# Performance work log

Hardware: AMD Instinct MI355X
Metric: run time of the kernel (lower is better)

Reference implementation:

```python
import jax, jax.numpy as jnp
import numpy as np

L, H, D, V, TMAX = 12, 12, 768, 50257, 1024
B, T = 2, 1024
HD = D // H
EPS = 1e-5


def new_gelu(x):
    return 0.5 * x * (1.0 + jnp.tanh(jnp.sqrt(2.0 / jnp.pi) * (x + 0.044715 * x ** 3)))


def layer_norm(x, w, b):
    mu = jnp.mean(x, axis=-1, keepdims=True)
    var = jnp.var(x, axis=-1, keepdims=True)
    return (x - mu) * jax.lax.rsqrt(var + EPS) * w + b


def setup_inputs() -> dict:
    key = jax.random.key(0)
    ks = jax.random.split(key, 12)
    s = 0.02
    return {
        "idx": jax.random.randint(ks[0], (B, T), 0, V),
        "wte": jax.random.normal(ks[1], (V, D), jnp.float32) * s,
        "wpe": jax.random.normal(ks[2], (TMAX, D), jnp.float32) * s,
        "ln1_w": jnp.ones((L, D), jnp.float32),
        "ln1_b": jnp.zeros((L, D), jnp.float32),
        "attn_w": jax.random.normal(ks[3], (L, D, 3 * D), jnp.float32) * s,
        "attn_b": jnp.zeros((L, 3 * D), jnp.float32),
        "proj_w": jax.random.normal(ks[4], (L, D, D), jnp.float32) * (s / jnp.sqrt(2.0 * L)),
        "proj_b": jnp.zeros((L, D), jnp.float32),
        "ln2_w": jnp.ones((L, D), jnp.float32),
        "ln2_b": jnp.zeros((L, D), jnp.float32),
        "fc_w": jax.random.normal(ks[5], (L, D, 4 * D), jnp.float32) * s,
        "fc_b": jnp.zeros((L, 4 * D), jnp.float32),
        "fc2_w": jax.random.normal(ks[6], (L, 4 * D, D), jnp.float32) * (s / jnp.sqrt(2.0 * L)),
        "fc2_b": jnp.zeros((L, D), jnp.float32),
        "lnf_w": jnp.ones((D,), jnp.float32),
        "lnf_b": jnp.zeros((D,), jnp.float32),
        "lm_head_w": jax.random.normal(ks[7], (D, V), jnp.float32) * s,
    }


def _gpt_forward(idx, wte, wpe, ln1_w, ln1_b, attn_w, attn_b, proj_w, proj_b,
                 ln2_w, ln2_b, fc_w, fc_b, fc2_w, fc2_b, lnf_w, lnf_b, lm_head_w):
    b, t = idx.shape
    x = wte[idx] + wpe[:t][None, :, :]  # [B,T,D]
    causal = jnp.tril(jnp.ones((t, t), bool))  # [T,T]
    scale = 1.0 / jnp.sqrt(jnp.asarray(HD, x.dtype))

    layer_params = {
        "ln1_w": ln1_w, "ln1_b": ln1_b, "attn_w": attn_w, "attn_b": attn_b,
        "proj_w": proj_w, "proj_b": proj_b, "ln2_w": ln2_w, "ln2_b": ln2_b,
        "fc_w": fc_w, "fc_b": fc_b, "fc2_w": fc2_w, "fc2_b": fc2_b,
    }

    def block(x, p):
        h = layer_norm(x, p["ln1_w"], p["ln1_b"])
        qkv = h @ p["attn_w"] + p["attn_b"]  # [B,T,3D]
        q, k, v = jnp.split(qkv, 3, axis=-1)
        q = q.reshape(b, t, H, HD)
        k = k.reshape(b, t, H, HD)
        v = v.reshape(b, t, H, HD)
        att = jnp.einsum("bqhd,bkhd->bhqk", q, k) * scale
        att = jnp.where(causal[None, None, :, :], att, -jnp.inf)
        att = jax.nn.softmax(att, axis=-1)
        y = jnp.einsum("bhqk,bkhd->bqhd", att, v).reshape(b, t, D)
        x = x + y @ p["proj_w"] + p["proj_b"]
        h2 = layer_norm(x, p["ln2_w"], p["ln2_b"])
        m = new_gelu(h2 @ p["fc_w"] + p["fc_b"])
        x = x + m @ p["fc2_w"] + p["fc2_b"]
        return x, None

    x, _ = jax.lax.scan(block, x, layer_params)
    x = layer_norm(x, lnf_w, lnf_b)
    logits = x @ lm_head_w  # [B,T,V]
    return logits


def reference(idx, wte, wpe, ln1_w, ln1_b, attn_w, attn_b, proj_w, proj_b,
              ln2_w, ln2_b, fc_w, fc_b, fc2_w, fc2_b, lnf_w, lnf_b, lm_head_w):
    return _gpt_forward(idx, wte, wpe, ln1_w, ln1_b, attn_w, attn_b, proj_w, proj_b,
                        ln2_w, ln2_b, fc_w, fc_b, fc2_w, fc2_b, lnf_w, lnf_b, lm_head_w)
```

## Files before the change

kernel.cpp:

```cpp
#include <hip/hip_runtime.h>
#include <math.h>

#define Bsz  2
#define Tlen 1024
#define Dm   768
#define Hh   12
#define HDm  64
#define Ll   12
#define Vv   50257
#define Mrows (Bsz * Tlen)
#define WPL  7077888

typedef __attribute__((ext_vector_type(8))) short short8;
typedef __attribute__((ext_vector_type(4))) float f32x4;

__device__ __forceinline__ float bf2f(unsigned short u) {
  union { unsigned int i; float f; } v; v.i = ((unsigned int)u) << 16; return v.f;
}
__device__ __forceinline__ unsigned short f2bf(float f) {
  union { float f; unsigned int i; } v; v.f = f;
  unsigned int u = v.i;
  return (unsigned short)((u + 0x7FFFu + ((u >> 16) & 1u)) >> 16);
}
__device__ __forceinline__ float gelu_f(float x) {
  const float c = 0.7978845608028654f;
  return 0.5f * x * (1.0f + tanhf(c * (x + 0.044715f * x * x * x)));
}

__device__ __forceinline__ void gl_lds16(const unsigned short* g, unsigned short* l) {
  __builtin_amdgcn_global_load_lds(
      (const __attribute__((address_space(1))) unsigned int*)g,
      (__attribute__((address_space(3))) unsigned int*)l, 16, 0, 0);
}


__global__ void embed_kernel(const int* __restrict__ idx, const float* __restrict__ wte,
                             const float* __restrict__ wpe, float* __restrict__ x) {
  int i = (blockIdx.x * 256 + threadIdx.x) * 4;
  int d = i % Dm;
  int bt = i / Dm;
  int t = bt % Tlen;
  int tok = idx[bt];
  float4 a = *(const float4*)(wte + (size_t)tok * Dm + d);
  float4 p = *(const float4*)(wpe + (size_t)t * Dm + d);
  float4 r; r.x = a.x + p.x; r.y = a.y + p.y; r.z = a.z + p.z; r.w = a.w + p.w;
  *(float4*)(x + i) = r;
}

__global__ __launch_bounds__(256) void ln_wave(const float* __restrict__ x,
                                               const float* __restrict__ w,
                                               const float* __restrict__ b,
                                               unsigned short* __restrict__ out) {
  int tid = threadIdx.x, wv = tid >> 6, l = tid & 63;
  int row = blockIdx.x * 4 + wv;
  const float* xr = x + (size_t)row * Dm;
  float4 v[3];
  float s = 0.f, s2 = 0.f;
#pragma unroll
  for (int i = 0; i < 3; ++i) {
    v[i] = *(const float4*)(xr + l * 4 + i * 256);
    s += v[i].x + v[i].y + v[i].z + v[i].w;
    s2 += v[i].x * v[i].x + v[i].y * v[i].y + v[i].z * v[i].z + v[i].w * v[i].w;
  }
#pragma unroll
  for (int o = 1; o < 64; o <<= 1) {
    s += __shfl_xor(s, o, 64);
    s2 += __shfl_xor(s2, o, 64);
  }
  float mu = s * (1.0f / Dm);
  float var = s2 * (1.0f / Dm) - mu * mu;
  float rstd = rsqrtf(var + 1e-5f);
  unsigned short* yr = out + (size_t)row * Dm;
#pragma unroll
  for (int i = 0; i < 3; ++i) {
    float4 wv4 = *(const float4*)(w + l * 4 + i * 256);
    float4 bv4 = *(const float4*)(b + l * 4 + i * 256);
    ushort4 o4;
    o4.x = f2bf((v[i].x - mu) * rstd * wv4.x + bv4.x);
    o4.y = f2bf((v[i].y - mu) * rstd * wv4.y + bv4.y);
    o4.z = f2bf((v[i].z - mu) * rstd * wv4.z + bv4.z);
    o4.w = f2bf((v[i].w - mu) * rstd * wv4.w + bv4.w);
    *(ushort4*)(yr + l * 4 + i * 256) = o4;
  }
}

__global__ __launch_bounds__(256) void tconv_kernel(const float* __restrict__ W, int ldw,
                                                    int nValid, unsigned short* __restrict__ WT,
                                                    int K) {
  __shared__ float S[32][33];
  int n0 = blockIdx.x * 32, k0 = blockIdx.y * 32;
  int t = threadIdx.x;
  int nc = t & 31, kr0 = t >> 5;
#pragma unroll
  for (int i = 0; i < 4; ++i) {
    int kr = kr0 + i * 8;
    S[kr][nc] = (n0 + nc < nValid) ? W[(size_t)(k0 + kr) * ldw + n0 + nc] : 0.f;
  }
  __syncthreads();
  int r = t >> 3, c4 = (t & 7) * 4;
  ushort4 o;
  o.x = f2bf(S[c4 + 0][r]); o.y = f2bf(S[c4 + 1][r]);
  o.z = f2bf(S[c4 + 2][r]); o.w = f2bf(S[c4 + 3][r]);
  *(ushort4*)(WT + (size_t)(n0 + r) * K + k0 + c4) = o;
}

__global__ __launch_bounds__(256) void tconv12_kernel(
    const float* __restrict__ attn_w, const float* __restrict__ proj_w,
    const float* __restrict__ fc_w, const float* __restrict__ fc2_w,
    unsigned short* __restrict__ wAll) {
  int bid = blockIdx.x;
  int lyr = bid / 6912, rem = bid % 6912;
  unsigned short* wL = wAll + (size_t)lyr * WPL;
  const float* W; unsigned short* WT; int ldw, K, ntn, local;
  if (rem < 1728)      { W = attn_w + (size_t)lyr * Dm * 3 * Dm; WT = wL;                     ldw = 2304; K = 768;  ntn = 72; local = rem; }
  else if (rem < 2304) { W = proj_w + (size_t)lyr * Dm * Dm;     WT = wL + 1769472;           ldw = 768;  K = 768;  ntn = 24; local = rem - 1728; }
  else if (rem < 4608) { W = fc_w + (size_t)lyr * Dm * 4 * Dm;   WT = wL + 1769472 + 589824;  ldw = 3072; K = 768;  ntn = 96; local = rem - 2304; }
  else                 { W = fc2_w + (size_t)lyr * 4 * Dm * Dm;  WT = wL + 1769472 + 589824 + 2359296; ldw = 768; K = 3072; ntn = 24; local = rem - 4608; }
  int n0 = (local % ntn) * 32, k0 = (local / ntn) * 32;
  __shared__ float S[32][33];
  int t = threadIdx.x;
  int nc = t & 31, kr0 = t >> 5;
#pragma unroll
  for (int i = 0; i < 4; ++i) {
    int kr = kr0 + i * 8;
    S[kr][nc] = W[(size_t)(k0 + kr) * ldw + n0 + nc];
  }
  __syncthreads();
  int r = t >> 3, c4 = (t & 7) * 4;
  ushort4 o;
  o.x = f2bf(S[c4 + 0][r]); o.y = f2bf(S[c4 + 1][r]);
  o.z = f2bf(S[c4 + 2][r]); o.w = f2bf(S[c4 + 3][r]);
  *(ushort4*)(WT + (size_t)(n0 + r) * K + k0 + c4) = o;
}

template<bool XMAP>
__global__ __launch_bounds__(256) void gemm_big(
    const unsigned short* __restrict__ A, const unsigned short* __restrict__ B, int K,
    const float* __restrict__ bias, const float* __restrict__ res,
    float* __restrict__ outF, unsigned short* __restrict__ outB,
    int ldc, int nValid, int act, int nColTiles) {
  int brow, bcol;
  if (XMAP) {
    int b = blockIdx.x, xcd = b & 7, slot = b >> 3;
    bcol = xcd + 8 * (slot >> 4);
    brow = slot & 15;
    if (bcol >= nColTiles) return;
  } else {
    bcol = blockIdx.x; brow = blockIdx.y;
  }
  __shared__ alignas(16) unsigned short As[3][128][32];
  __shared__ alignas(16) unsigned short Bs[3][128][32];
  int tid = threadIdx.x;
  int rowBase = brow * 128, colBase = bcol * 128;
  int w = tid >> 6, l = tid & 63;
  int wr = w >> 1, wc = w & 1;
  int srow = tid >> 2;
  int skk = (((tid & 3) ^ ((tid >> 3) & 3))) * 8;
  const unsigned short* aSrc = A + (size_t)(rowBase + srow) * K + skk;
  const unsigned short* bSrc = B + (size_t)(colBase + srow) * K + skk;

  f32x4 acc[4][4];
#pragma unroll
  for (int m = 0; m < 4; ++m)
#pragma unroll
    for (int n = 0; n < 4; ++n) acc[m][n] = (f32x4){0.f, 0.f, 0.f, 0.f};

  int fr = l & 15, fq = l >> 4;
  int kslot = (fq ^ ((fr >> 1) & 3)) * 8;

#define STAGE_BIG(t_, buf_)                                              \
  { int k0_ = (t_) * 32;                                                 \
    gl_lds16(aSrc + k0_, &As[buf_][w * 16][0]);                          \
    gl_lds16(aSrc + (size_t)64 * K + k0_, &As[buf_][w * 16 + 64][0]);    \
    gl_lds16(bSrc + k0_, &Bs[buf_][w * 16][0]);                          \
    gl_lds16(bSrc + (size_t)64 * K + k0_, &Bs[buf_][w * 16 + 64][0]); }

  int nIt = K >> 5;
  STAGE_BIG(0, 0);
  STAGE_BIG(1, 1);

  int cur = 0;
  for (int it = 0; it < nIt; ++it) {
    if (it + 2 < nIt) {
      int nxt = cur + 2; if (nxt >= 3) nxt -= 3;
      STAGE_BIG(it + 2, nxt);
      asm volatile("s_waitcnt vmcnt(8)" ::: "memory");
    } else if (it + 1 < nIt) {
      asm volatile("s_waitcnt vmcnt(4)" ::: "memory");
    } else {
      asm volatile("s_waitcnt vmcnt(0)" ::: "memory");
    }
    asm volatile("s_barrier" ::: "memory");

    short8 af[4], bfr[4];
#pragma unroll
    for (int m = 0; m < 4; ++m)
      af[m] = *(const short8*)&As[cur][wr * 64 + m * 16 + fr][kslot];
#pragma unroll
    for (int n = 0; n < 4; ++n)
      bfr[n] = *(const short8*)&Bs[cur][wc * 64 + n * 16 + fr][kslot];
#pragma unroll
    for (int m = 0; m < 4; ++m)
#pragma unroll
      for (int n = 0; n < 4; ++n)
        acc[m][n] = __builtin_amdgcn_mfma_f32_16x16x32_bf16(af[m], bfr[n], acc[m][n], 0, 0, 0);
    asm volatile("s_barrier" ::: "memory");
    cur = cur + 1; if (cur >= 3) cur = 0;
  }
#undef STAGE_BIG

#pragma unroll
  for (int m = 0; m < 4; ++m) {
    int row = rowBase + wr * 64 + m * 16 + fq * 4;
#pragma unroll
    for (int n = 0; n < 4; ++n) {
      int col = colBase + wc * 64 + n * 16 + fr;
      if (col >= nValid) continue;
      float bv = bias ? bias[col] : 0.f;
#pragma unroll
      for (int j = 0; j < 4; ++j) {
        float v = acc[m][n][j] + bv;
        if (act) v = gelu_f(v);
        if (res) v += res[(size_t)(row + j) * ldc + col];
        if (outF) outF[(size_t)(row + j) * ldc + col] = v;
        else      outB[(size_t)(row + j) * ldc + col] = f2bf(v);
      }
    }
  }
}

__global__ __launch_bounds__(256) void gemm_bf16_sm(
    const unsigned short* __restrict__ A, const unsigned short* __restrict__ B, int K,
    const float* __restrict__ bias,
    float* __restrict__ outF, unsigned short* __restrict__ outB,
    int ldc, int act) {
  __shared__ alignas(16) unsigned short As[3][64][32];
  __shared__ alignas(16) unsigned short Bs[3][128][32];
  int tid = threadIdx.x;
  int rowBase = blockIdx.y * 64;
  int colBase = blockIdx.x * 128;
  int w = tid >> 6, l = tid & 63;
  int fr = l & 15, fq = l >> 4;

  int srow = l >> 2;
  int skk = (((l & 3) ^ ((l >> 3) & 3))) * 8;
  const unsigned short* aSrc = A + (size_t)(rowBase + w * 16 + srow) * K + skk;
  const unsigned short* bSrc = B + (size_t)(colBase + w * 16 + srow) * K + skk;
  int kslot = (fq ^ ((fr >> 1) & 3)) * 8;

  f32x4 acc[4][2];
#pragma unroll
  for (int m = 0; m < 4; ++m)
#pragma unroll
    for (int n = 0; n < 2; ++n) acc[m][n] = (f32x4){0.f, 0.f, 0.f, 0.f};

#define STAGE_SM(t_, buf_)                                               \
  { int k0_ = (t_) * 32;                                                 \
    gl_lds16(aSrc + k0_, &As[buf_][w * 16][0]);                          \
    gl_lds16(bSrc + k0_, &Bs[buf_][w * 16][0]);                          \
    gl_lds16(bSrc + (size_t)64 * K + k0_, &Bs[buf_][w * 16 + 64][0]); }

  int nIt = K >> 5;
  STAGE_SM(0, 0);
  STAGE_SM(1, 1);

  int cur = 0;
  for (int it = 0; it < nIt; ++it) {
    if (it + 2 < nIt) {
      int nxt = cur + 2; if (nxt >= 3) nxt -= 3;
      STAGE_SM(it + 2, nxt);
      asm volatile("s_waitcnt vmcnt(6)" ::: "memory");
    } else if (it + 1 < nIt) {
      asm volatile("s_waitcnt vmcnt(3)" ::: "memory");
    } else {
      asm volatile("s_waitcnt vmcnt(0)" ::: "memory");
    }
    asm volatile("s_barrier" ::: "memory");

    short8 af[4], bfr[2];
#pragma unroll
    for (int m = 0; m < 4; ++m)
      af[m] = *(const short8*)&As[cur][m * 16 + fr][kslot];
#pragma unroll
    for (int n = 0; n < 2; ++n)
      bfr[n] = *(const short8*)&Bs[cur][w * 32 + n * 16 + fr][kslot];
#pragma unroll
    for (int m = 0; m < 4; ++m)
#pragma unroll
      for (int n = 0; n < 2; ++n)
        acc[m][n] = __builtin_amdgcn_mfma_f32_16x16x32_bf16(af[m], bfr[n], acc[m][n], 0, 0, 0);
    asm volatile("s_barrier" ::: "memory");
    cur = cur + 1; if (cur >= 3) cur = 0;
  }
#undef STAGE_SM

#pragma unroll
  for (int m = 0; m < 4; ++m) {
    int row = rowBase + m * 16 + fq * 4;
#pragma unroll
    for (int n = 0; n < 2; ++n) {
      int col = colBase + w * 32 + n * 16 + fr;
      float bv = bias ? bias[col] : 0.f;
#pragma unroll
      for (int j = 0; j < 4; ++j) {
        float v = acc[m][n][j] + bv;
        if (act) v = gelu_f(v);
        if (outF) outF[(size_t)(row + j) * ldc + col] = v;
        else      outB[(size_t)(row + j) * ldc + col] = f2bf(v);
      }
    }
  }
}

__global__ __launch_bounds__(256) void gemm_splitk(
    const unsigned short* __restrict__ A, const unsigned short* __restrict__ B, int K,
    int Klen, const float* __restrict__ bias, float* __restrict__ outF, int ldc) {
  __shared__ alignas(16) unsigned short As[3][64][32];
  __shared__ alignas(16) unsigned short Bs[3][128][32];
  int tid = threadIdx.x;
  int rowBase = blockIdx.y * 64;
  int colBase = blockIdx.x * 128;
  int Koff = blockIdx.z * Klen;
  int w = tid >> 6, l = tid & 63;
  int fr = l & 15, fq = l >> 4;

  int srow = l >> 2;
  int skk = (((l & 3) ^ ((l >> 3) & 3))) * 8;
  const unsigned short* aSrc = A + (size_t)(rowBase + w * 16 + srow) * K + Koff + skk;
  const unsigned short* bSrc = B + (size_t)(colBase + w * 16 + srow) * K + Koff + skk;
  int kslot = (fq ^ ((fr >> 1) & 3)) * 8;

  f32x4 acc[4][2];
#pragma unroll
  for (int m = 0; m < 4; ++m)
#pragma unroll
    for (int n = 0; n < 2; ++n) acc[m][n] = (f32x4){0.f, 0.f, 0.f, 0.f};

#define STAGE_SK(t_, buf_)                                               \
  { int k0_ = (t_) * 32;                                                 \
    gl_lds16(aSrc + k0_, &As[buf_][w * 16][0]);                          \
    gl_lds16(bSrc + k0_, &Bs[buf_][w * 16][0]);                          \
    gl_lds16(bSrc + (size_t)64 * K + k0_, &Bs[buf_][w * 16 + 64][0]); }

  int nIt = Klen >> 5;
  STAGE_SK(0, 0);
  STAGE_SK(1, 1);

  int cur = 0;
  for (int it = 0; it < nIt; ++it) {
    if (it + 2 < nIt) {
      int nxt = cur + 2; if (nxt >= 3) nxt -= 3;
      STAGE_SK(it + 2, nxt);
      asm volatile("s_waitcnt vmcnt(6)" ::: "memory");
    } else if (it + 1 < nIt) {
      asm volatile("s_waitcnt vmcnt(3)" ::: "memory");
    } else {
      asm volatile("s_waitcnt vmcnt(0)" ::: "memory");
    }
    asm volatile("s_barrier" ::: "memory");

    short8 af[4], bfr[2];
#pragma unroll
    for (int m = 0; m < 4; ++m)
      af[m] = *(const short8*)&As[cur][m * 16 + fr][kslot];
#pragma unroll
    for (int n = 0; n < 2; ++n)
      bfr[n] = *(const short8*)&Bs[cur][w * 32 + n * 16 + fr][kslot];
#pragma unroll
    for (int m = 0; m < 4; ++m)
#pragma unroll
      for (int n = 0; n < 2; ++n)
        acc[m][n] = __builtin_amdgcn_mfma_f32_16x16x32_bf16(af[m], bfr[n], acc[m][n], 0, 0, 0);
    asm volatile("s_barrier" ::: "memory");
    cur = cur + 1; if (cur >= 3) cur = 0;
  }
#undef STAGE_SK

  bool addBias = (blockIdx.z == 0);
#pragma unroll
  for (int m = 0; m < 4; ++m) {
    int row = rowBase + m * 16 + fq * 4;
#pragma unroll
    for (int n = 0; n < 2; ++n) {
      int col = colBase + w * 32 + n * 16 + fr;
      float bv = addBias ? bias[col] : 0.f;
#pragma unroll
      for (int j = 0; j < 4; ++j) {
        unsafeAtomicAdd(&outF[(size_t)(row + j) * ldc + col], acc[m][n][j] + bv);
      }
    }
  }
}

__global__ __launch_bounds__(256) void attn_mfma(const unsigned short* __restrict__ qkv,
                                                 unsigned short* __restrict__ y) {
  int bx = blockIdx.x;
  int qt = 15 - (bx / 24);
  int bh = bx % 24;
  int h  = bh % Hh;
  int b  = bh / Hh;
  int q0 = qt * 64;
  int tid = threadIdx.x;
  int w = tid >> 6, l = tid & 63;
  int g = l >> 4, fr = l & 15;

  __shared__ alignas(16) unsigned short Kl[2][4096];
  __shared__ alignas(16) unsigned short Vt[4096];
  __shared__ alignas(16) unsigned short Pl[4][1024];

  const size_t rs = 3 * Dm;
  const unsigned short* base = qkv + (size_t)(b * Tlen) * rs + h * HDm;

  short8 qf[2];
  {
    const unsigned short* qrow = base + (size_t)(q0 + w * 16 + fr) * rs;
    qf[0] = *(const short8*)(qrow + g * 8);
    qf[1] = *(const short8*)(qrow + g * 8 + 32);
  }

  int vt_t = tid >> 2, vt_dc = tid & 3;
  uint4 v0r, v1r;

  f32x4 oAcc[4];
#pragma unroll
  for (int nd = 0; nd < 4; ++nd) oAcc[nd] = (f32x4){0.f, 0.f, 0.f, 0.f};
  float mRun[4] = {-1e30f, -1e30f, -1e30f, -1e30f};
  float lRun[4] = {0.f, 0.f, 0.f, 0.f};

  unsigned short* Pw = &Pl[w][0];
  int nkt = qt + 1;

  {
#pragma unroll
    for (int i = 0; i < 2; ++i) {
      int c = i * 256 + tid;
      int t = c >> 3, cl = c & 7;
      int dch = cl ^ (t & 7);
      gl_lds16(base + (size_t)t * rs + Dm + dch * 8, &Kl[0][(i * 256 + w * 64) * 8]);
    }
    const unsigned short* p = base + (size_t)vt_t * rs + 2 * Dm + vt_dc * 16;
    v0r = *(const uint4*)p;
    v1r = *(const uint4*)(p + 8);
  }

  for (int kt = 0; kt < nkt; ++kt) {
    int cur = kt & 1;
    int kbase = kt * 64;
    asm volatile("s_waitcnt vmcnt(0)" ::: "memory");
    __builtin_amdgcn_s_barrier();

    {
      union { uint4 u; unsigned short s[8]; } a, bb;
      a.u = v0r; bb.u = v1r;
#pragma unroll
      for (int j = 0; j < 8; ++j) {
        int d = vt_dc * 16 + j;
        Vt[d * 64 + (vt_t ^ ((d & 7) << 3))] = a.s[j];
        int d2 = d + 8;
        Vt[d2 * 64 + (vt_t ^ ((d2 & 7) << 3))] = bb.s[j];
      }
    }
    if (kt + 1 < nkt) {
      int kb = kbase + 64;
#pragma unroll
      for (int i = 0; i < 2; ++i) {
        int c = i * 256 + tid;
        int t = c >> 3, cl = c & 7;
        int dch = cl ^ (t & 7);
        gl_lds16(base + (size_t)(kb + t) * rs + Dm + dch * 8,
                 &Kl[cur ^ 1][(i * 256 + w * 64) * 8]);
      }
      const unsigned short* p = base + (size_t)(kb + vt_t) * rs + 2 * Dm + vt_dc * 16;
      v0r = *(const uint4*)p;
      v1r = *(const uint4*)(p + 8);
    }
    asm volatile("s_waitcnt lgkmcnt(0)" ::: "memory");
    __builtin_amdgcn_s_barrier();

    f32x4 sAcc[4];
#pragma unroll
    for (int nt = 0; nt < 4; ++nt) sAcc[nt] = (f32x4){0.f, 0.f, 0.f, 0.f};
#pragma unroll
    for (int ks = 0; ks < 2; ++ks)
#pragma unroll
      for (int nt = 0; nt < 4; ++nt) {
        int kcol = nt * 16 + fr;
        short8 kf = *(const short8*)&Kl[cur][kcol * 64 + ((g * 8 + ks * 32) ^ ((kcol & 7) << 3))];
        sAcc[nt] = __builtin_amdgcn_mfma_f32_16x16x32_bf16(qf[ks], kf, sAcc[nt], 0, 0, 0);
      }

    float corr[4];
#pragma unroll
    for (int j = 0; j < 4; ++j) {
      int qg = q0 + w * 16 + g * 4 + j;
      float tm = -1e30f;
#pragma unroll
      for (int nt = 0; nt < 4; ++nt) {
        float s = sAcc[nt][j] * 0.125f;
        int tg = kbase + nt * 16 + fr;
        if (tg > qg) s = -1e30f;
        sAcc[nt][j] = s;
        tm = fmaxf(tm, s);
      }
      tm = fmaxf(tm, __shfl_xor(tm, 1, 16));
      tm = fmaxf(tm, __shfl_xor(tm, 2, 16));
      tm = fmaxf(tm, __shfl_xor(tm, 4, 16));
      tm = fmaxf(tm, __shfl_xor(tm, 8, 16));
      float mN = fmaxf(mRun[j], tm);
      corr[j] = __expf(mRun[j] - mN);
      mRun[j] = mN;
      float ps = 0.f;
#pragma unroll
      for (int nt = 0; nt < 4; ++nt) {
        float p = __expf(sAcc[nt][j] - mN);
        sAcc[nt][j] = p;
        ps += p;
      }
      ps += __shfl_xor(ps, 1, 16);
      ps += __shfl_xor(ps, 2, 16);
      ps += __shfl_xor(ps, 4, 16);
      ps += __shfl_xor(ps, 8, 16);
      lRun[j] = lRun[j] * corr[j] + ps;
    }

#pragma unroll
    for (int nt = 0; nt < 4; ++nt)
#pragma unroll
      for (int j = 0; j < 4; ++j) {
        int q = g * 4 + j;
        int t = nt * 16 + fr;
        Pw[q * 64 + (t ^ ((q & 7) << 3))] = f2bf(sAcc[nt][j]);
      }
#pragma unroll
    for (int nd = 0; nd < 4; ++nd)
#pragma unroll
      for (int j = 0; j < 4; ++j) oAcc[nd][j] *= corr[j];

#pragma unroll
    for (int ks = 0; ks < 2; ++ks) {
      short8 pf = *(const short8*)&Pw[fr * 64 + ((g * 8 + ks * 32) ^ ((fr & 7) << 3))];
#pragma unroll
      for (int nd = 0; nd < 4; ++nd) {
        int d = nd * 16 + fr;
        short8 vf = *(const short8*)&Vt[d * 64 + ((g * 8 + ks * 32) ^ ((fr & 7) << 3))];
        oAcc[nd] = __builtin_amdgcn_mfma_f32_16x16x32_bf16(pf, vf, oAcc[nd], 0, 0, 0);
      }
    }
  }

#pragma unroll
  for (int j = 0; j < 4; ++j) {
    float inv = 1.0f / lRun[j];
    int q = q0 + w * 16 + g * 4 + j;
    unsigned short* yr = y + (size_t)(b * Tlen + q) * Dm + h * HDm + fr;
#pragma unroll
    for (int nd = 0; nd < 4; ++nd)
      yr[nd * 16] = f2bf(oAcc[nd][j] * inv);
  }
}

extern "C" void kernel_launch(void* const* d_in, const int* in_sizes, int n_in,
                              void* d_out, int out_size, void* d_ws, size_t ws_size,
                              hipStream_t stream) {
  const int*   idx    = (const int*)d_in[0];
  const float* wte    = (const float*)d_in[1];
  const float* wpe    = (const float*)d_in[2];
  const float* ln1_w  = (const float*)d_in[3];
  const float* ln1_b  = (const float*)d_in[4];
  const float* attn_w = (const float*)d_in[5];
  const float* attn_b = (const float*)d_in[6];
  const float* proj_w = (const float*)d_in[7];
  const float* proj_b = (const float*)d_in[8];
  const float* ln2_w  = (const float*)d_in[9];
  const float* ln2_b  = (const float*)d_in[10];
  const float* fc_w   = (const float*)d_in[11];
  const float* fc_b   = (const float*)d_in[12];
  const float* fc2_w  = (const float*)d_in[13];
  const float* fc2_b  = (const float*)d_in[14];
  const float* lnf_w  = (const float*)d_in[15];
  const float* lnf_b  = (const float*)d_in[16];
  const float* lmw    = (const float*)d_in[17];
  float* out = (float*)d_out;

  float* x = (float*)d_ws;
  unsigned short* qkvb = (unsigned short*)(x + (size_t)Mrows * Dm);
  unsigned short* xb   = qkvb + (size_t)Mrows * 3 * Dm;
  unsigned short* yb   = xb + (size_t)Mrows * Dm;
  unsigned short* mb   = yb + (size_t)Mrows * Dm;
  unsigned short* wbuf = mb + (size_t)Mrows * 4 * Dm;

  unsigned short* wAll = (unsigned short*)d_out;

  const size_t baseBytes = (size_t)Mrows * Dm * 4 + (size_t)Mrows * 9 * Dm * 2;
  size_t availShorts = (ws_size - baseBytes) / 2;
  long long cc = (long long)(availShorts / Dm) & ~127LL;
  if (cc > 50304) cc = 50304;
  const int chunkCols = (int)cc;

  embed_kernel<<<(Mrows * Dm) / 1024, 256, 0, stream>>>(idx, wte, wpe, x);
  tconv12_kernel<<<6912 * Ll, 256, 0, stream>>>(attn_w, proj_w, fc_w, fc2_w, wAll);

  for (int l = 0; l < Ll; ++l) {
    unsigned short* wL    = wAll + (size_t)l * WPL;
    unsigned short* wAttn = wL;
    unsigned short* wProj = wL + 1769472;
    unsigned short* wFc   = wL + 1769472 + 589824;
    unsigned short* wFc2  = wL + 1769472 + 589824 + 2359296;

    ln_wave<<<Mrows / 4, 256, 0, stream>>>(x, ln1_w + l * Dm, ln1_b + l * Dm, xb);
    gemm_bf16_sm<<<dim3(18, 32), 256, 0, stream>>>(xb, wAttn, Dm, attn_b + (size_t)l * 3 * Dm,
                                                   nullptr, qkvb, 3 * Dm, 0);
    attn_mfma<<<Bsz * Hh * 16, 256, 0, stream>>>(qkvb, yb);
    gemm_splitk<<<dim3(6, 32, 2), 256, 0, stream>>>(yb, wProj, Dm, Dm / 2,
                                                    proj_b + (size_t)l * Dm, x, Dm);
    ln_wave<<<Mrows / 4, 256, 0, stream>>>(x, ln2_w + l * Dm, ln2_b + l * Dm, xb);
    gemm_bf16_sm<<<dim3(24, 32), 256, 0, stream>>>(xb, wFc, Dm, fc_b + (size_t)l * 4 * Dm,
                                                   nullptr, mb, 4 * Dm, 1);
    gemm_splitk<<<dim3(6, 32, 2), 256, 0, stream>>>(mb, wFc2, 4 * Dm, 2 * Dm,
                                                    fc2_b + (size_t)l * Dm, x, Dm);
  }

  ln_wave<<<Mrows / 4, 256, 0, stream>>>(x, lnf_w, lnf_b, xb);
  for (int base = 0; base < Vv; base += chunkCols) {
    int ncv = Vv - base; if (ncv > chunkCols) ncv = chunkCols;
    int ntiles = (ncv + 127) / 128;
    tconv_kernel<<<dim3((ncv + 31) / 32, 24), 256, 0, stream>>>(lmw + base, Vv, ncv, wbuf, Dm);
    int cpx = (ntiles + 7) / 8;
    gemm_big<true><<<8 * 16 * cpx, 256, 0, stream>>>(
        xb, wbuf, Dm, nullptr, nullptr, out + base, nullptr, Vv, ncv, 0, ntiles);
  }
}
```

Before: 2.228 ms.

## Split causal attention over key ranges with merge kernel; single-barrier GEMM pipelines

```diff
diff --git a/kernel.cpp b/kernel.cpp
--- a/kernel.cpp
+++ b/kernel.cpp
@@ -181,16 +181,13 @@
 
   int cur = 0;
   for (int it = 0; it < nIt; ++it) {
+    if (it < nIt - 1) asm volatile("s_waitcnt vmcnt(4)" ::: "memory");
+    else              asm volatile("s_waitcnt vmcnt(0)" ::: "memory");
+    asm volatile("s_barrier" ::: "memory");
     if (it + 2 < nIt) {
       int nxt = cur + 2; if (nxt >= 3) nxt -= 3;
       STAGE_BIG(it + 2, nxt);
-      asm volatile("s_waitcnt vmcnt(8)" ::: "memory");
-    } else if (it + 1 < nIt) {
-      asm volatile("s_waitcnt vmcnt(4)" ::: "memory");
-    } else {
-      asm volatile("s_waitcnt vmcnt(0)" ::: "memory");
-    }
-    asm volatile("s_barrier" ::: "memory");
+    }
 
     short8 af[4], bfr[4];
 #pragma unroll
@@ -204,7 +201,6 @@
 #pragma unroll
       for (int n = 0; n < 4; ++n)
         acc[m][n] = __builtin_amdgcn_mfma_f32_16x16x32_bf16(af[m], bfr[n], acc[m][n], 0, 0, 0);
-    asm volatile("s_barrier" ::: "memory");
     cur = cur + 1; if (cur >= 3) cur = 0;
   }
 #undef STAGE_BIG
@@ -266,16 +262,13 @@
 
   int cur = 0;
   for (int it = 0; it < nIt; ++it) {
+    if (it < nIt - 1) asm volatile("s_waitcnt vmcnt(3)" ::: "memory");
+    else              asm volatile("s_waitcnt vmcnt(0)" ::: "memory");
+    asm volatile("s_barrier" ::: "memory");
     if (it + 2 < nIt) {
       int nxt = cur + 2; if (nxt >= 3) nxt -= 3;
       STAGE_SM(it + 2, nxt);
-      asm volatile("s_waitcnt vmcnt(6)" ::: "memory");
-    } else if (it + 1 < nIt) {
-      asm volatile("s_waitcnt vmcnt(3)" ::: "memory");
-    } else {
-      asm volatile("s_waitcnt vmcnt(0)" ::: "memory");
-    }
-    asm volatile("s_barrier" ::: "memory");
+    }
 
     short8 af[4], bfr[2];
 #pragma unroll
@@ -289,7 +282,6 @@
 #pragma unroll
       for (int n = 0; n < 2; ++n)
         acc[m][n] = __builtin_amdgcn_mfma_f32_16x16x32_bf16(af[m], bfr[n], acc[m][n], 0, 0, 0);
-    asm volatile("s_barrier" ::: "memory");
     cur = cur + 1; if (cur >= 3) cur = 0;
   }
 #undef STAGE_SM
@@ -348,16 +340,13 @@
 
   int cur = 0;
   for (int it = 0; it < nIt; ++it) {
+    if (it < nIt - 1) asm volatile("s_waitcnt vmcnt(3)" ::: "memory");
+    else              asm volatile("s_waitcnt vmcnt(0)" ::: "memory");
+    asm volatile("s_barrier" ::: "memory");
     if (it + 2 < nIt) {
       int nxt = cur + 2; if (nxt >= 3) nxt -= 3;
       STAGE_SK(it + 2, nxt);
-      asm volatile("s_waitcnt vmcnt(6)" ::: "memory");
-    } else if (it + 1 < nIt) {
-      asm volatile("s_waitcnt vmcnt(3)" ::: "memory");
-    } else {
-      asm volatile("s_waitcnt vmcnt(0)" ::: "memory");
-    }
-    asm volatile("s_barrier" ::: "memory");
+    }
 
     short8 af[4], bfr[2];
 #pragma unroll
@@ -371,7 +360,6 @@
 #pragma unroll
       for (int n = 0; n < 2; ++n)
         acc[m][n] = __builtin_amdgcn_mfma_f32_16x16x32_bf16(af[m], bfr[n], acc[m][n], 0, 0, 0);
-    asm volatile("s_barrier" ::: "memory");
     cur = cur + 1; if (cur >= 3) cur = 0;
   }
 #undef STAGE_SK
@@ -393,12 +381,21 @@
 }
 
 __global__ __launch_bounds__(256) void attn_mfma(const unsigned short* __restrict__ qkv,
-                                                 unsigned short* __restrict__ y) {
-  int bx = blockIdx.x;
-  int qt = 15 - (bx / 24);
-  int bh = bx % 24;
-  int h  = bh % Hh;
-  int b  = bh / Hh;
+                                                 unsigned short* __restrict__ y,
+                                                 float* __restrict__ pO,
+                                                 float* __restrict__ pML) {
+  int bh = blockIdx.y;
+  int h = bh % Hh, b = bh / Hh;
+  int u = blockIdx.x, qt = 0, sp = 0;
+  for (int q = 15; q >= 0; --q) {
+    int ns = (q + 4) >> 2;
+    if (u < ns) { qt = q; sp = u; break; }
+    u -= ns;
+  }
+  int nsp = (qt + 4) >> 2;
+  int ktBeg = sp * 4;
+  int ktEnd = min(ktBeg + 4, qt + 1);
+
   int q0 = qt * 64;
   int tid = threadIdx.x;
   int w = tid >> 6, l = tid & 63;
@@ -428,7 +425,6 @@
   float lRun[4] = {0.f, 0.f, 0.f, 0.f};
 
   unsigned short* Pw = &Pl[w][0];
-  int nkt = qt + 1;
 
   {
 #pragma unroll
@@ -436,15 +432,16 @@
       int c = i * 256 + tid;
       int t = c >> 3, cl = c & 7;
       int dch = cl ^ (t & 7);
-      gl_lds16(base + (size_t)t * rs + Dm + dch * 8, &Kl[0][(i * 256 + w * 64) * 8]);
-    }
-    const unsigned short* p = base + (size_t)vt_t * rs + 2 * Dm + vt_dc * 16;
+      gl_lds16(base + (size_t)(ktBeg * 64 + t) * rs + Dm + dch * 8,
+               &Kl[0][(i * 256 + w * 64) * 8]);
+    }
+    const unsigned short* p = base + (size_t)(ktBeg * 64 + vt_t) * rs + 2 * Dm + vt_dc * 16;
     v0r = *(const uint4*)p;
     v1r = *(const uint4*)(p + 8);
   }
 
-  for (int kt = 0; kt < nkt; ++kt) {
-    int cur = kt & 1;
+  for (int kt = ktBeg; kt < ktEnd; ++kt) {
+    int cur = (kt - ktBeg) & 1;
     int kbase = kt * 64;
     asm volatile("s_waitcnt vmcnt(0)" ::: "memory");
     __builtin_amdgcn_s_barrier();
@@ -460,7 +457,7 @@
         Vt[d2 * 64 + (vt_t ^ ((d2 & 7) << 3))] = bb.s[j];
       }
     }
-    if (kt + 1 < nkt) {
+    if (kt + 1 < ktEnd) {
       int kb = kbase + 64;
 #pragma unroll
       for (int i = 0; i < 2; ++i) {
@@ -548,15 +545,79 @@
     }
   }
 
-#pragma unroll
-  for (int j = 0; j < 4; ++j) {
-    float inv = 1.0f / lRun[j];
-    int q = q0 + w * 16 + g * 4 + j;
-    unsigned short* yr = y + (size_t)(b * Tlen + q) * Dm + h * HDm + fr;
-#pragma unroll
-    for (int nd = 0; nd < 4; ++nd)
-      yr[nd * 16] = f2bf(oAcc[nd][j] * inv);
-  }
+  if (nsp == 1) {
+#pragma unroll
+    for (int j = 0; j < 4; ++j) {
+      float inv = 1.0f / lRun[j];
+      int q = q0 + w * 16 + g * 4 + j;
+      unsigned short* yr = y + (size_t)(b * Tlen + q) * Dm + h * HDm + fr;
+#pragma unroll
+      for (int nd = 0; nd < 4; ++nd)
+        yr[nd * 16] = f2bf(oAcc[nd][j] * inv);
+    }
+  } else {
+    int sb = 0;
+    for (int uq = 4; uq < qt; ++uq) sb += (uq + 4) >> 2;
+    int slot = bh * 36 + sb + sp;
+    float* po = pO + (size_t)slot * 4096;
+    float* pml = pML + (size_t)slot * 128;
+#pragma unroll
+    for (int j = 0; j < 4; ++j) {
+      int q = w * 16 + g * 4 + j;
+#pragma unroll
+      for (int nd = 0; nd < 4; ++nd)
+        po[q * 64 + nd * 16 + fr] = oAcc[nd][j];
+      if (fr == 0) {
+        pml[q] = mRun[j];
+        pml[64 + q] = lRun[j];
+      }
+    }
+  }
+}
+
+__global__ __launch_bounds__(256) void attn_merge(const float* __restrict__ pO,
+                                                  const float* __restrict__ pML,
+                                                  unsigned short* __restrict__ y) {
+  int qt = 4 + blockIdx.x;
+  int bh = blockIdx.y;
+  int h = bh % Hh, b = bh / Hh;
+  int nsp = (qt + 4) >> 2;
+  int sb = 0;
+  for (int uq = 4; uq < qt; ++uq) sb += (uq + 4) >> 2;
+  int slot0 = bh * 36 + sb;
+
+  int t = threadIdx.x;
+  int q = t >> 2, dg = t & 3, d0 = dg * 16;
+
+  float m[4], lv[4];
+  float M = -1e30f;
+  for (int i = 0; i < nsp; ++i) {
+    m[i] = pML[(size_t)(slot0 + i) * 128 + q];
+    lv[i] = pML[(size_t)(slot0 + i) * 128 + 64 + q];
+    M = fmaxf(M, m[i]);
+  }
+  float L = 0.f;
+  float od[16];
+#pragma unroll
+  for (int k = 0; k < 16; ++k) od[k] = 0.f;
+  for (int i = 0; i < nsp; ++i) {
+    float wgt = __expf(m[i] - M);
+    L += wgt * lv[i];
+    const float* po = pO + (size_t)(slot0 + i) * 4096 + q * 64 + d0;
+#pragma unroll
+    for (int k = 0; k < 16; k += 4) {
+      float4 v = *(const float4*)(po + k);
+      od[k] += wgt * v.x; od[k + 1] += wgt * v.y;
+      od[k + 2] += wgt * v.z; od[k + 3] += wgt * v.w;
+    }
+  }
+  float inv = 1.0f / L;
+  union { uint4 u[2]; unsigned short s[16]; } pk;
+#pragma unroll
+  for (int k = 0; k < 16; ++k) pk.s[k] = f2bf(od[k] * inv);
+  unsigned short* yr = y + (size_t)(b * Tlen + qt * 64 + q) * Dm + h * HDm + d0;
+  *(uint4*)yr = pk.u[0];
+  *(uint4*)(yr + 8) = pk.u[1];
 }
 
 extern "C" void kernel_launch(void* const* d_in, const int* in_sizes, int n_in,
@@ -590,6 +651,8 @@
   unsigned short* wbuf = mb + (size_t)Mrows * 4 * Dm;
 
   unsigned short* wAll = (unsigned short*)d_out;
+  float* pO  = (float*)(wAll + (size_t)12 * WPL);
+  float* pML = pO + (size_t)864 * 4096;
 
   const size_t baseBytes = (size_t)Mrows * Dm * 4 + (size_t)Mrows * 9 * Dm * 2;
   size_t availShorts = (ws_size - baseBytes) / 2;
@@ -610,7 +673,8 @@
     ln_wave<<<Mrows / 4, 256, 0, stream>>>(x, ln1_w + l * Dm, ln1_b + l * Dm, xb);
     gemm_bf16_sm<<<dim3(18, 32), 256, 0, stream>>>(xb, wAttn, Dm, attn_b + (size_t)l * 3 * Dm,
                                                    nullptr, qkvb, 3 * Dm, 0);
-    attn_mfma<<<Bsz * Hh * 16, 256, 0, stream>>>(qkvb, yb);
+    attn_mfma<<<dim3(40, 24), 256, 0, stream>>>(qkvb, yb, pO, pML);
+    attn_merge<<<dim3(12, 24), 256, 0, stream>>>(pO, pML, yb);
     gemm_splitk<<<dim3(6, 32, 2), 256, 0, stream>>>(yb, wProj, Dm, Dm / 2,
                                                     proj_b + (size_t)l * Dm, x, Dm);
     ln_wave<<<Mrows / 4, 256, 0, stream>>>(x, ln2_w + l * Dm, ln2_b + l * Dm, xb);
```

Result: no change. 2.238 ms (+0.5%).
